# Optimization experiments

Measured on AMD Instinct MI355X. Metric: run time of the kernel, lower is better.

Reference implementation:

```python
import jax, jax.numpy as jnp
import numpy as np

EMBED_DIM = 1024
NUM_HEADS = 16
HEAD_DIM = EMBED_DIM // NUM_HEADS
TGT_LEN, BSZ = 2048, 4


def setup_inputs() -> dict:
    key = jax.random.key(0)
    ks = jax.random.split(key, 12)
    s = 1.0 / np.sqrt(EMBED_DIM)
    inp = {
        "query": jax.random.normal(ks[0], (TGT_LEN, BSZ, EMBED_DIM), jnp.float32),
        "key": jax.random.normal(ks[1], (TGT_LEN, BSZ, EMBED_DIM), jnp.float32),
        "value": jax.random.normal(ks[2], (TGT_LEN, BSZ, EMBED_DIM), jnp.float32),
        # nn.Linear weights: [out, in], y = x @ W.T + b
        "Wq": jax.random.normal(ks[3], (EMBED_DIM, EMBED_DIM), jnp.float32) * s,
        "bq": jax.random.normal(ks[4], (EMBED_DIM,), jnp.float32) * s,
        "Wk": jax.random.normal(ks[5], (EMBED_DIM, EMBED_DIM), jnp.float32) * s,
        "bk": jax.random.normal(ks[6], (EMBED_DIM,), jnp.float32) * s,
        "Wv": jax.random.normal(ks[7], (EMBED_DIM, EMBED_DIM), jnp.float32) * s,
        "bv": jax.random.normal(ks[8], (EMBED_DIM,), jnp.float32) * s,
        "Wo": jax.random.normal(ks[9], (EMBED_DIM, EMBED_DIM), jnp.float32) * s,
        "bo": jax.random.normal(ks[10], (EMBED_DIM,), jnp.float32) * s,
    }
    return inp


def _split_heads(x, seq_len, bsz):
    # [S, B, E] -> [B*H, S, Dh]
    return x.reshape(seq_len, bsz * NUM_HEADS, HEAD_DIM).transpose(1, 0, 2)


def reference(query, key, value, Wq, bq, Wk, bk, Wv, bv, Wo, bo):
    tgt_len, bsz, embed_dim = query.shape
    src_len = key.shape[0]
    q = query @ Wq.T + bq
    k = key @ Wk.T + bk
    v = value @ Wv.T + bv
    q = _split_heads(q, tgt_len, bsz)   # [B*H, T, Dh]
    k = _split_heads(k, src_len, bsz)   # [B*H, S, Dh]
    v = _split_heads(v, src_len, bsz)   # [B*H, S, Dh]
    scale = 1.0 / np.sqrt(HEAD_DIM).astype(np.float32)
    attn_weights = jnp.einsum('btd,bsd->bts', q, k) * scale  # [B*H, T, S]
    attn_weights = jax.nn.softmax(attn_weights, axis=-1)
    attn = jnp.einsum('bts,bsd->btd', attn_weights, v)       # [B*H, T, Dh]
    attn = attn.transpose(1, 0, 2).reshape(tgt_len, bsz, embed_dim)
    return attn @ Wo.T + bo
```

## Files before the change

kernel.cpp:

```cpp
#include <hip/hip_runtime.h>
#include <stdint.h>

#define TGT 2048
#define BSZQ 4
#define EMB 1024
#define NHEAD 16
#define DH 64
#define BH 64
#define MROWS 8192

using short8 = __attribute__((ext_vector_type(8))) short;
using f32x4  = __attribute__((ext_vector_type(4))) float;
typedef unsigned short u16;
typedef unsigned int u32;

#define QSCALE 0.18033688011112042f

__device__ __forceinline__ u16 f2bf(float f) {
  union { float f; u32 u; } v; v.f = f;
  return (u16)((v.u + 0x7fffu + ((v.u >> 16) & 1u)) >> 16);
}
__device__ __forceinline__ u32 packbf(float a, float b) {
  union { float f; u32 u; } x, y; x.f = a; y.f = b;
  return __builtin_amdgcn_perm(y.u + 0x8000u, x.u + 0x8000u, 0x07060302u);
}
__device__ __forceinline__ f32x4 mfma16(short8 a, short8 b, f32x4 c) {
  return __builtin_amdgcn_mfma_f32_16x16x32_bf16(a, b, c, 0, 0, 0);
}
__device__ __forceinline__ void gload_lds16(const u16* g, u16* l) {
  __builtin_amdgcn_global_load_lds((const __attribute__((address_space(1))) void*)g,
                                   (__attribute__((address_space(3))) void*)l,
                                   16, 0, 0);
}

__global__ __launch_bounds__(256)
void cvt3(const float* __restrict__ a, const float* __restrict__ b, const float* __restrict__ c,
          u16* __restrict__ oa, u16* __restrict__ ob, u16* __restrict__ oc)
{
  const float* s; u16* d;
  if (blockIdx.y == 0) { s = a; d = oa; }
  else if (blockIdx.y == 1) { s = b; d = ob; }
  else { s = c; d = oc; }
  const int i = (blockIdx.x * 256 + threadIdx.x) * 8;
  float4 v0 = *(const float4*)(s + i);
  float4 v1 = *(const float4*)(s + i + 4);
  union { u16 h[8]; short8 v; } r;
  r.h[0] = f2bf(v0.x); r.h[1] = f2bf(v0.y); r.h[2] = f2bf(v0.z); r.h[3] = f2bf(v0.w);
  r.h[4] = f2bf(v1.x); r.h[5] = f2bf(v1.y); r.h[6] = f2bf(v1.z); r.h[7] = f2bf(v1.w);
  *(short8*)(d + i) = r.v;
}
__global__ __launch_bounds__(256)
void cvt4(const float* __restrict__ a, const float* __restrict__ b,
          const float* __restrict__ c, const float* __restrict__ e,
          u16* __restrict__ oa, u16* __restrict__ ob, u16* __restrict__ oc, u16* __restrict__ oe)
{
  const float* s; u16* d;
  if (blockIdx.y == 0) { s = a; d = oa; }
  else if (blockIdx.y == 1) { s = b; d = ob; }
  else if (blockIdx.y == 2) { s = c; d = oc; }
  else { s = e; d = oe; }
  const int i = (blockIdx.x * 256 + threadIdx.x) * 8;
  float4 v0 = *(const float4*)(s + i);
  float4 v1 = *(const float4*)(s + i + 4);
  union { u16 h[8]; short8 v; } r;
  r.h[0] = f2bf(v0.x); r.h[1] = f2bf(v0.y); r.h[2] = f2bf(v0.z); r.h[3] = f2bf(v0.w);
  r.h[4] = f2bf(v1.x); r.h[5] = f2bf(v1.y); r.h[6] = f2bf(v1.z); r.h[7] = f2bf(v1.w);
  *(short8*)(d + i) = r.v;
}

__device__ __forceinline__
void gemm_body(const u16* __restrict__ A, const u16* __restrict__ W,
               const float* __restrict__ bias, void* __restrict__ outp,
               u16* As, u16* Bs, int mode, int m0, int n0)
{
  const int tid = threadIdx.x;
  const int wave = tid >> 6, lane = tid & 63;
  const int col16 = lane & 15, quad = lane >> 4;
  const int wr = (wave >> 1) * 64;
  const int wc = (wave & 1) * 64;
  const int sr = lane >> 3;
  const int sg = (lane & 7) ^ sr;
  const int fk = col16 & 7;

#define GSTAGE(K0) do { \
  _Pragma("unroll") for (int s_ = 0; s_ < 4; ++s_) \
    gload_lds16(A + (size_t)(m0 + wave * 32 + s_ * 8 + sr) * EMB + (K0) + sg * 8, \
                &As[(wave * 32 + s_ * 8) * 64]); \
  _Pragma("unroll") for (int s_ = 0; s_ < 4; ++s_) \
    gload_lds16(W + (size_t)(n0 + wave * 32 + s_ * 8 + sr) * EMB + (K0) + sg * 8, \
                &Bs[(wave * 32 + s_ * 8) * 64]); \
} while (0)

  f32x4 acc[4][4];
#pragma unroll
  for (int i = 0; i < 4; ++i)
#pragma unroll
    for (int j = 0; j < 4; ++j) acc[i][j] = (f32x4)0.0f;

  for (int kt = 0; kt < EMB / 64; ++kt) {
    if (kt) __syncthreads();
    GSTAGE(kt * 64);
    __syncthreads();
    short8 af[4][2], bfr[4][2];
#pragma unroll
    for (int kk = 0; kk < 2; ++kk) {
#pragma unroll
      for (int i = 0; i < 4; ++i)
        af[i][kk] = *(const short8*)&As[(wr + i * 16 + col16) * 64
                                        + (((kk * 4 + quad) ^ fk) << 3)];
#pragma unroll
      for (int j = 0; j < 4; ++j)
        bfr[j][kk] = *(const short8*)&Bs[(wc + j * 16 + col16) * 64
                                         + (((kk * 4 + quad) ^ fk) << 3)];
    }
#pragma unroll
    for (int i = 0; i < 4; ++i)
#pragma unroll
      for (int j = 0; j < 4; ++j) {
        acc[i][j] = mfma16(af[i][0], bfr[j][0], acc[i][j]);
        acc[i][j] = mfma16(af[i][1], bfr[j][1], acc[i][j]);
      }
  }
#undef GSTAGE

  const int rowb = quad * 4;
#pragma unroll
  for (int i = 0; i < 4; ++i) {
#pragma unroll
    for (int j = 0; j < 4; ++j) {
      const int gn = n0 + wc + j * 16 + col16;
      const float bia = bias[gn];
      const int h = gn >> 6, d = gn & 63;
#pragma unroll
      for (int r = 0; r < 4; ++r) {
        const int gm = m0 + wr + i * 16 + rowb + r;
        float val = acc[i][j][r] + bia;
        const int t = gm >> 2, b = gm & 3;
        if (mode == 0) {
          ((u16*)outp)[((size_t)(b * NHEAD + h) * TGT + t) * DH + d] = f2bf(val * QSCALE);
        } else if (mode == 1) {
          ((u16*)outp)[((size_t)(b * NHEAD + h) * TGT + t) * DH + d] = f2bf(val);
        } else if (mode == 2) {
          const int p = (t & ~63) + ((t & 12) << 2) + ((t & 48) >> 2) + (t & 3);
          ((u16*)outp)[((size_t)(b * NHEAD + h) * DH + d) * TGT + p] = f2bf(val);
        } else {
          ((float*)outp)[(size_t)gm * EMB + gn] = val;
        }
      }
    }
  }
}

__global__ __launch_bounds__(256, 4)
void gemm_qkv(const u16* __restrict__ qb, const u16* __restrict__ kb, const u16* __restrict__ vb,
              const u16* __restrict__ wq, const u16* __restrict__ wk, const u16* __restrict__ wv,
              const float* __restrict__ bq, const float* __restrict__ bk, const float* __restrict__ bv,
              u16* __restrict__ qh, u16* __restrict__ kh, u16* __restrict__ vtp)
{
  __shared__ u16 As[8192];
  __shared__ u16 Bs[8192];
  const int lin = ((int)blockIdx.z * 64 + blockIdx.y) * 8 + blockIdx.x;
  const int swz = (lin & 7) * 192 + (lin >> 3);
  const int n0 = (swz & 7) * 128;
  const int tmp = swz >> 3;
  const int m0 = (tmp & 63) * 128;
  const int z = tmp >> 6;
  const u16* A = (z == 0) ? qb : (z == 1) ? kb : vb;
  const u16* W = (z == 0) ? wq : (z == 1) ? wk : wv;
  const float* bias = (z == 0) ? bq : (z == 1) ? bk : bv;
  void* outp = (z == 0) ? (void*)qh : (z == 1) ? (void*)kh : (void*)vtp;
  gemm_body(A, W, bias, outp, As, Bs, z, m0, n0);
}

__global__ __launch_bounds__(256, 4)
void gemm_o(const u16* __restrict__ A, const u16* __restrict__ W,
            const float* __restrict__ bias, float* __restrict__ outp)
{
  __shared__ u16 As[8192];
  __shared__ u16 Bs[8192];
  const int lin = (int)blockIdx.y * 8 + blockIdx.x;
  const int swz = (lin & 7) * 64 + (lin >> 3);
  const int n0 = (swz & 7) * 128;
  const int m0 = (swz >> 3) * 128;
  gemm_body(A, W, bias, (void*)outp, As, Bs, 3, m0, n0);
}

__global__ __launch_bounds__(256, 4)
void flash_attn(const u16* __restrict__ qh, const u16* __restrict__ kh,
                const u16* __restrict__ vtp, u16* __restrict__ ao)
{
  __shared__ u16 Ks[2 * 64 * 64];
  __shared__ u16 Vs[2 * 64 * 64];

  const int tid = threadIdx.x;
  const int wave = tid >> 6, lane = tid & 63;
  const int col16 = lane & 15, quad = lane >> 4;
  const int id = blockIdx.x;
  const int bh = (id & 7) * 8 + (id >> 7);
  const int q0 = ((id >> 3) & 15) * 128;
  const int wq0 = q0 + wave * 32;

  const u16* qbase = qh + (size_t)bh * TGT * DH;
  const u16* kbase = kh + (size_t)bh * TGT * DH;
  const u16* vbase = vtp + (size_t)bh * DH * TGT;

  const int krl = lane >> 3;
  const int kgl = (lane & 7) ^ krl;

#define STAGE(S0, B) do { \
  _Pragma("unroll") for (int t_ = 0; t_ < 2; ++t_) { \
    gload_lds16(kbase + (size_t)((S0) + t_ * 32 + wave * 8 + krl) * DH + kgl * 8, \
                &Ks[(B) * 4096 + (t_ * 32 + wave * 8) * 64]); \
    gload_lds16(vbase + (size_t)(t_ * 32 + wave * 8 + krl) * TGT + (S0) + kgl * 8, \
                &Vs[(B) * 4096 + (t_ * 32 + wave * 8) * 64]); \
  } } while (0)

  short8 qf[2][2];
#pragma unroll
  for (int i = 0; i < 2; ++i)
#pragma unroll
    for (int kk = 0; kk < 2; ++kk)
      qf[i][kk] = *(const short8*)(qbase + (size_t)(wq0 + i * 16 + col16) * DH + kk * 32 + quad * 8);

  f32x4 oacc[2][4];
  float lsum[2];
#pragma unroll
  for (int i = 0; i < 2; ++i) {
    lsum[i] = 0.0f;
#pragma unroll
    for (int j = 0; j < 4; ++j) oacc[i][j] = (f32x4)0.0f;
  }

  STAGE(0, 0);

  for (int st = 0; st < TGT / 64; ++st) {
    const int cb = st & 1;
    __syncthreads();
    if (st < TGT / 64 - 1) STAGE((st + 1) * 64, cb ^ 1);

    u32 pka[4][2][2];
#pragma unroll
    for (int j = 0; j < 4; ++j) {
      const int R = j * 16 + col16;
      short8 kf0 = *(const short8*)&Ks[cb * 4096 + R * 64 + ((quad ^ (col16 & 7)) << 3)];
      short8 kf1 = *(const short8*)&Ks[cb * 4096 + R * 64 + (((quad + 4) ^ (col16 & 7)) << 3)];
#pragma unroll
      for (int i = 0; i < 2; ++i) {
        f32x4 t0 = mfma16(kf0, qf[i][0], (f32x4)0.0f);
        f32x4 s  = mfma16(kf1, qf[i][1], t0);
        float p0 = __builtin_amdgcn_exp2f(s[0]);
        float p1 = __builtin_amdgcn_exp2f(s[1]);
        float p2 = __builtin_amdgcn_exp2f(s[2]);
        float p3 = __builtin_amdgcn_exp2f(s[3]);
        lsum[i] += (p0 + p1) + (p2 + p3);
        pka[j][i][0] = packbf(p0, p1);
        pka[j][i][1] = packbf(p2, p3);
      }
    }
#pragma unroll
    for (int jd = 0; jd < 4; ++jd) {
      const int d = jd * 16 + col16;
#pragma unroll
      for (int h = 0; h < 2; ++h) {
        short8 vf = *(const short8*)&Vs[cb * 4096 + d * 64
                                        + (((quad * 2 + h) ^ (d & 7)) << 3)];
#pragma unroll
        for (int i = 0; i < 2; ++i) {
          union { u32 u[4]; short8 s8; } pa;
          pa.u[0] = pka[2 * h][i][0];     pa.u[1] = pka[2 * h][i][1];
          pa.u[2] = pka[2 * h + 1][i][0]; pa.u[3] = pka[2 * h + 1][i][1];
          oacc[i][jd] = mfma16(pa.s8, vf, oacc[i][jd]);
        }
      }
    }
  }
#undef STAGE

  float lrow[2][4];
#pragma unroll
  for (int i = 0; i < 2; ++i) {
    float L = lsum[i];
    L += __shfl_xor(L, 16, 64);
    L += __shfl_xor(L, 32, 64);
    L = __builtin_amdgcn_rcpf(L);
#pragma unroll
    for (int r = 0; r < 4; ++r) lrow[i][r] = __shfl(L, quad * 4 + r, 64);
  }
  const int b = bh >> 4, h = bh & 15;
#pragma unroll
  for (int i = 0; i < 2; ++i)
#pragma unroll
    for (int jd = 0; jd < 4; ++jd)
#pragma unroll
      for (int r = 0; r < 4; ++r) {
        const int t = q0 + wave * 32 + i * 16 + quad * 4 + r;
        const int d = jd * 16 + col16;
        ao[((size_t)t * BSZQ + b) * EMB + h * DH + d] = f2bf(oacc[i][jd][r] * lrow[i][r]);
      }
}

extern "C" void kernel_launch(void* const* d_in, const int* in_sizes, int n_in,
                              void* d_out, int out_size, void* d_ws, size_t ws_size,
                              hipStream_t stream) {
  const float* query = (const float*)d_in[0];
  const float* key   = (const float*)d_in[1];
  const float* value = (const float*)d_in[2];
  const float* Wq = (const float*)d_in[3];
  const float* bq = (const float*)d_in[4];
  const float* Wk = (const float*)d_in[5];
  const float* bk = (const float*)d_in[6];
  const float* Wv = (const float*)d_in[7];
  const float* bv = (const float*)d_in[8];
  const float* Wo = (const float*)d_in[9];
  const float* bo = (const float*)d_in[10];

  const size_t BIG = (size_t)MROWS * EMB;
  const size_t WSZ = (size_t)EMB * EMB;
  u16* buf0 = (u16*)d_ws;
  u16* buf1 = buf0 + BIG;
  u16* buf2 = buf1 + BIG;
  u16* buf3 = buf2 + BIG;
  u16* wqb  = buf3 + BIG;
  u16* wkb  = wqb + WSZ;
  u16* wvb  = wkb + WSZ;
  u16* wob  = wvb + WSZ;
  u16* khs  = (u16*)d_out;
  u16* vts  = khs + BIG;

  cvt3<<<dim3(BIG / 2048, 3), 256, 0, stream>>>(query, key, value, buf0, buf1, buf2);
  cvt4<<<dim3(WSZ / 2048, 4), 256, 0, stream>>>(Wq, Wk, Wv, Wo, wqb, wkb, wvb, wob);

  gemm_qkv<<<dim3(EMB / 128, MROWS / 128, 3), 256, 0, stream>>>(
      buf0, buf1, buf2, wqb, wkb, wvb, bq, bk, bv,
      buf3 , khs , vts );

  flash_attn<<<1024, 256, 0, stream>>>(buf3, khs, vts, buf2);

  gemm_o<<<dim3(EMB / 128, MROWS / 128), 256, 0, stream>>>(buf2, wob, bo, (float*)d_out);
}
```

Baseline: 360.2 us.

## Double-buffer GEMM LDS tiles with K=32 stages and fragment-ordered layout

The shared GEMM body now splits K into 32-wide stages held in two LDS buffers. It issues the global-to-LDS load for the next stage before computing the current one, so each iteration needs one barrier instead of two. The LDS layout changes from XOR-swizzled 64-wide rows to 16x32 fragment-ordered blocks, so each lane reads its MFMA operand directly without swizzle arithmetic. This costs twice as many loop iterations with half the MFMAs each. The new read pattern may also behave differently for bank conflicts, and correctness depends on the async load completing before the barrier.

```diff
diff --git a/kernel.cpp b/kernel.cpp
--- a/kernel.cpp
+++ b/kernel.cpp
@@ -78,18 +78,19 @@
   const int col16 = lane & 15, quad = lane >> 4;
   const int wr = (wave >> 1) * 64;
   const int wc = (wave & 1) * 64;
-  const int sr = lane >> 3;
-  const int sg = (lane & 7) ^ sr;
-  const int fk = col16 & 7;
-
-#define GSTAGE(K0) do { \
-  _Pragma("unroll") for (int s_ = 0; s_ < 4; ++s_) \
-    gload_lds16(A + (size_t)(m0 + wave * 32 + s_ * 8 + sr) * EMB + (K0) + sg * 8, \
-                &As[(wave * 32 + s_ * 8) * 64]); \
-  _Pragma("unroll") for (int s_ = 0; s_ < 4; ++s_) \
-    gload_lds16(W + (size_t)(n0 + wave * 32 + s_ * 8 + sr) * EMB + (K0) + sg * 8, \
-                &Bs[(wave * 32 + s_ * 8) * 64]); \
-} while (0)
+  const int sr16 = lane & 15;
+  const int sl = lane >> 4;
+  const int akb = (wave >> 1) * 4;
+  const int bkb = (wave & 1) * 4;
+
+#define GSTAGE(K0, CB) do { \
+  _Pragma("unroll") for (int s_ = 0; s_ < 2; ++s_) { \
+    const int t_ = wave * 2 + s_; \
+    gload_lds16(A + (size_t)(m0 + t_ * 16 + sr16) * EMB + (K0) + sl * 8, \
+                &As[(CB) * 4096 + t_ * 512]); \
+    gload_lds16(W + (size_t)(n0 + t_ * 16 + sr16) * EMB + (K0) + sl * 8, \
+                &Bs[(CB) * 4096 + t_ * 512]); \
+  } } while (0)
 
   f32x4 acc[4][4];
 #pragma unroll
@@ -97,29 +98,23 @@
 #pragma unroll
     for (int j = 0; j < 4; ++j) acc[i][j] = (f32x4)0.0f;
 
-  for (int kt = 0; kt < EMB / 64; ++kt) {
-    if (kt) __syncthreads();
-    GSTAGE(kt * 64);
+  GSTAGE(0, 0);
+  for (int kt = 0; kt < EMB / 32; ++kt) {
+    const int cb = kt & 1;
     __syncthreads();
-    short8 af[4][2], bfr[4][2];
-#pragma unroll
-    for (int kk = 0; kk < 2; ++kk) {
-#pragma unroll
-      for (int i = 0; i < 4; ++i)
-        af[i][kk] = *(const short8*)&As[(wr + i * 16 + col16) * 64
-                                        + (((kk * 4 + quad) ^ fk) << 3)];
+    if (kt < EMB / 32 - 1) GSTAGE((kt + 1) * 32, cb ^ 1);
+    short8 af[4], bfr[4];
+#pragma unroll
+    for (int i = 0; i < 4; ++i)
+      af[i] = *(const short8*)&As[cb * 4096 + (akb + i) * 512 + quad * 128 + col16 * 8];
+#pragma unroll
+    for (int j = 0; j < 4; ++j)
+      bfr[j] = *(const short8*)&Bs[cb * 4096 + (bkb + j) * 512 + quad * 128 + col16 * 8];
+#pragma unroll
+    for (int i = 0; i < 4; ++i)
 #pragma unroll
       for (int j = 0; j < 4; ++j)
-        bfr[j][kk] = *(const short8*)&Bs[(wc + j * 16 + col16) * 64
-                                         + (((kk * 4 + quad) ^ fk) << 3)];
-    }
-#pragma unroll
-    for (int i = 0; i < 4; ++i)
-#pragma unroll
-      for (int j = 0; j < 4; ++j) {
-        acc[i][j] = mfma16(af[i][0], bfr[j][0], acc[i][j]);
-        acc[i][j] = mfma16(af[i][1], bfr[j][1], acc[i][j]);
-      }
+        acc[i][j] = mfma16(af[i], bfr[j], acc[i][j]);
   }
 #undef GSTAGE
 
@@ -157,8 +152,8 @@
               const float* __restrict__ bq, const float* __restrict__ bk, const float* __restrict__ bv,
               u16* __restrict__ qh, u16* __restrict__ kh, u16* __restrict__ vtp)
 {
-  __shared__ u16 As[8192];
-  __shared__ u16 Bs[8192];
+  __shared__ u16 As[2 * 4096];
+  __shared__ u16 Bs[2 * 4096];
   const int lin = ((int)blockIdx.z * 64 + blockIdx.y) * 8 + blockIdx.x;
   const int swz = (lin & 7) * 192 + (lin >> 3);
   const int n0 = (swz & 7) * 128;
@@ -176,8 +171,8 @@
 void gemm_o(const u16* __restrict__ A, const u16* __restrict__ W,
             const float* __restrict__ bias, float* __restrict__ outp)
 {
-  __shared__ u16 As[8192];
-  __shared__ u16 Bs[8192];
+  __shared__ u16 As[2 * 4096];
+  __shared__ u16 Bs[2 * 4096];
   const int lin = (int)blockIdx.y * 8 + blockIdx.x;
   const int swz = (lin & 7) * 64 + (lin >> 3);
   const int n0 = (swz & 7) * 128;
```

New measurement: 404.2 us. +12.2%, slower.

## Use 256x128 QKV GEMM tiles with 512 threads and merge conversion kernels

Applied to the files above, without the earlier changes.

Merges the two fp32-to-bf16 conversion kernels into one launch, with weight blocks beyond their size exiting early. The QKV projection GEMM moves to 256x128 tiles with 8 waves per block, halving the block count and reusing each staged weight tile across more rows. Its LDS layout changes to 16-row sub-tiles without the XOR swizzle, which may bring bank conflicts back. The larger block also uses more LDS and drops the 4-blocks-per-CU launch bound, which can lower occupancy.

```diff
diff --git a/kernel.cpp b/kernel.cpp
--- a/kernel.cpp
+++ b/kernel.cpp
@@ -34,95 +34,38 @@
 }
 
 __global__ __launch_bounds__(256)
-void cvt3(const float* __restrict__ a, const float* __restrict__ b, const float* __restrict__ c,
-          u16* __restrict__ oa, u16* __restrict__ ob, u16* __restrict__ oc)
-{
+void cvt_all(const float* __restrict__ q, const float* __restrict__ k, const float* __restrict__ v,
+             const float* __restrict__ wq, const float* __restrict__ wk,
+             const float* __restrict__ wv, const float* __restrict__ wo,
+             u16* __restrict__ oq, u16* __restrict__ ok, u16* __restrict__ ov,
+             u16* __restrict__ owq, u16* __restrict__ owk, u16* __restrict__ owv,
+             u16* __restrict__ owo)
+{
+  const int y = blockIdx.y;
+  if (y >= 3 && blockIdx.x >= 512) return;
   const float* s; u16* d;
-  if (blockIdx.y == 0) { s = a; d = oa; }
-  else if (blockIdx.y == 1) { s = b; d = ob; }
-  else { s = c; d = oc; }
+  switch (y) {
+    case 0: s = q;  d = oq;  break;
+    case 1: s = k;  d = ok;  break;
+    case 2: s = v;  d = ov;  break;
+    case 3: s = wq; d = owq; break;
+    case 4: s = wk; d = owk; break;
+    case 5: s = wv; d = owv; break;
+    default: s = wo; d = owo; break;
+  }
   const int i = (blockIdx.x * 256 + threadIdx.x) * 8;
   float4 v0 = *(const float4*)(s + i);
   float4 v1 = *(const float4*)(s + i + 4);
-  union { u16 h[8]; short8 v; } r;
+  union { u16 h[8]; short8 vv; } r;
   r.h[0] = f2bf(v0.x); r.h[1] = f2bf(v0.y); r.h[2] = f2bf(v0.z); r.h[3] = f2bf(v0.w);
   r.h[4] = f2bf(v1.x); r.h[5] = f2bf(v1.y); r.h[6] = f2bf(v1.z); r.h[7] = f2bf(v1.w);
-  *(short8*)(d + i) = r.v;
-}
-__global__ __launch_bounds__(256)
-void cvt4(const float* __restrict__ a, const float* __restrict__ b,
-          const float* __restrict__ c, const float* __restrict__ e,
-          u16* __restrict__ oa, u16* __restrict__ ob, u16* __restrict__ oc, u16* __restrict__ oe)
-{
-  const float* s; u16* d;
-  if (blockIdx.y == 0) { s = a; d = oa; }
-  else if (blockIdx.y == 1) { s = b; d = ob; }
-  else if (blockIdx.y == 2) { s = c; d = oc; }
-  else { s = e; d = oe; }
-  const int i = (blockIdx.x * 256 + threadIdx.x) * 8;
-  float4 v0 = *(const float4*)(s + i);
-  float4 v1 = *(const float4*)(s + i + 4);
-  union { u16 h[8]; short8 v; } r;
-  r.h[0] = f2bf(v0.x); r.h[1] = f2bf(v0.y); r.h[2] = f2bf(v0.z); r.h[3] = f2bf(v0.w);
-  r.h[4] = f2bf(v1.x); r.h[5] = f2bf(v1.y); r.h[6] = f2bf(v1.z); r.h[7] = f2bf(v1.w);
-  *(short8*)(d + i) = r.v;
+  *(short8*)(d + i) = r.vv;
 }
 
 __device__ __forceinline__
-void gemm_body(const u16* __restrict__ A, const u16* __restrict__ W,
-               const float* __restrict__ bias, void* __restrict__ outp,
-               u16* As, u16* Bs, int mode, int m0, int n0)
-{
-  const int tid = threadIdx.x;
-  const int wave = tid >> 6, lane = tid & 63;
-  const int col16 = lane & 15, quad = lane >> 4;
-  const int wr = (wave >> 1) * 64;
-  const int wc = (wave & 1) * 64;
-  const int sr = lane >> 3;
-  const int sg = (lane & 7) ^ sr;
-  const int fk = col16 & 7;
-
-#define GSTAGE(K0) do { \
-  _Pragma("unroll") for (int s_ = 0; s_ < 4; ++s_) \
-    gload_lds16(A + (size_t)(m0 + wave * 32 + s_ * 8 + sr) * EMB + (K0) + sg * 8, \
-                &As[(wave * 32 + s_ * 8) * 64]); \
-  _Pragma("unroll") for (int s_ = 0; s_ < 4; ++s_) \
-    gload_lds16(W + (size_t)(n0 + wave * 32 + s_ * 8 + sr) * EMB + (K0) + sg * 8, \
-                &Bs[(wave * 32 + s_ * 8) * 64]); \
-} while (0)
-
-  f32x4 acc[4][4];
-#pragma unroll
-  for (int i = 0; i < 4; ++i)
-#pragma unroll
-    for (int j = 0; j < 4; ++j) acc[i][j] = (f32x4)0.0f;
-
-  for (int kt = 0; kt < EMB / 64; ++kt) {
-    if (kt) __syncthreads();
-    GSTAGE(kt * 64);
-    __syncthreads();
-    short8 af[4][2], bfr[4][2];
-#pragma unroll
-    for (int kk = 0; kk < 2; ++kk) {
-#pragma unroll
-      for (int i = 0; i < 4; ++i)
-        af[i][kk] = *(const short8*)&As[(wr + i * 16 + col16) * 64
-                                        + (((kk * 4 + quad) ^ fk) << 3)];
-#pragma unroll
-      for (int j = 0; j < 4; ++j)
-        bfr[j][kk] = *(const short8*)&Bs[(wc + j * 16 + col16) * 64
-                                         + (((kk * 4 + quad) ^ fk) << 3)];
-    }
-#pragma unroll
-    for (int i = 0; i < 4; ++i)
-#pragma unroll
-      for (int j = 0; j < 4; ++j) {
-        acc[i][j] = mfma16(af[i][0], bfr[j][0], acc[i][j]);
-        acc[i][j] = mfma16(af[i][1], bfr[j][1], acc[i][j]);
-      }
-  }
-#undef GSTAGE
-
+void gemm_epilogue(f32x4 acc[4][4], const float* __restrict__ bias, void* __restrict__ outp,
+                   int mode, int m0, int n0, int wr, int wc, int col16, int quad)
+{
   const int rowb = quad * 4;
 #pragma unroll
   for (int i = 0; i < 4; ++i) {
@@ -151,25 +94,79 @@
   }
 }
 
-__global__ __launch_bounds__(256, 4)
+__global__ __launch_bounds__(512)
 void gemm_qkv(const u16* __restrict__ qb, const u16* __restrict__ kb, const u16* __restrict__ vb,
               const u16* __restrict__ wq, const u16* __restrict__ wk, const u16* __restrict__ wv,
               const float* __restrict__ bq, const float* __restrict__ bk, const float* __restrict__ bv,
               u16* __restrict__ qh, u16* __restrict__ kh, u16* __restrict__ vtp)
 {
-  __shared__ u16 As[8192];
+  __shared__ u16 As[16384];
   __shared__ u16 Bs[8192];
-  const int lin = ((int)blockIdx.z * 64 + blockIdx.y) * 8 + blockIdx.x;
-  const int swz = (lin & 7) * 192 + (lin >> 3);
+
+  const int lin = ((int)blockIdx.z * 32 + blockIdx.y) * 8 + blockIdx.x;
+  const int swz = (lin & 7) * 96 + (lin >> 3);
   const int n0 = (swz & 7) * 128;
   const int tmp = swz >> 3;
-  const int m0 = (tmp & 63) * 128;
-  const int z = tmp >> 6;
+  const int m0 = (tmp & 31) * 256;
+  const int z = tmp >> 5;
   const u16* A = (z == 0) ? qb : (z == 1) ? kb : vb;
   const u16* W = (z == 0) ? wq : (z == 1) ? wk : wv;
   const float* bias = (z == 0) ? bq : (z == 1) ? bk : bv;
   void* outp = (z == 0) ? (void*)qh : (z == 1) ? (void*)kh : (void*)vtp;
-  gemm_body(A, W, bias, outp, As, Bs, z, m0, n0);
+
+  const int tid = threadIdx.x;
+  const int wave = tid >> 6, lane = tid & 63;
+  const int col16 = lane & 15, quad = lane >> 4;
+  const int wr = (wave >> 1) * 64;
+  const int wc = (wave & 1) * 64;
+  const int sr = lane & 15;
+  const int sq = lane >> 4;
+
+#define GSTAGE(K0) do { \
+  _Pragma("unroll") for (int g_ = 0; g_ < 2; ++g_) { \
+    const int t_ = wave * 2 + g_; \
+    _Pragma("unroll") for (int h_ = 0; h_ < 2; ++h_) \
+      gload_lds16(A + (size_t)(m0 + t_ * 16 + sr) * EMB + (K0) + (h_ * 4 + sq) * 8, \
+                  &As[t_ * 1024 + h_ * 512]); \
+  } \
+  _Pragma("unroll") for (int h_ = 0; h_ < 2; ++h_) \
+    gload_lds16(W + (size_t)(n0 + wave * 16 + sr) * EMB + (K0) + (h_ * 4 + sq) * 8, \
+                &Bs[wave * 1024 + h_ * 512]); \
+} while (0)
+
+  f32x4 acc[4][4];
+#pragma unroll
+  for (int i = 0; i < 4; ++i)
+#pragma unroll
+    for (int j = 0; j < 4; ++j) acc[i][j] = (f32x4)0.0f;
+
+  for (int kt = 0; kt < EMB / 64; ++kt) {
+    if (kt) __syncthreads();
+    GSTAGE(kt * 64);
+    __syncthreads();
+    short8 af[4][2], bfr[4][2];
+#pragma unroll
+    for (int kk = 0; kk < 2; ++kk) {
+#pragma unroll
+      for (int i = 0; i < 4; ++i)
+        af[i][kk] = *(const short8*)&As[((wave >> 1) * 4 + i) * 1024
+                                        + ((kk * 4 + quad) * 16 + col16) * 8];
+#pragma unroll
+      for (int j = 0; j < 4; ++j)
+        bfr[j][kk] = *(const short8*)&Bs[((wave & 1) * 4 + j) * 1024
+                                         + ((kk * 4 + quad) * 16 + col16) * 8];
+    }
+#pragma unroll
+    for (int i = 0; i < 4; ++i)
+#pragma unroll
+      for (int j = 0; j < 4; ++j) {
+        acc[i][j] = mfma16(af[i][0], bfr[j][0], acc[i][j]);
+        acc[i][j] = mfma16(af[i][1], bfr[j][1], acc[i][j]);
+      }
+  }
+#undef GSTAGE
+
+  gemm_epilogue(acc, bias, outp, z, m0, n0, wr, wc, col16, quad);
 }
 
 __global__ __launch_bounds__(256, 4)
@@ -182,7 +179,58 @@
   const int swz = (lin & 7) * 64 + (lin >> 3);
   const int n0 = (swz & 7) * 128;
   const int m0 = (swz >> 3) * 128;
-  gemm_body(A, W, bias, (void*)outp, As, Bs, 3, m0, n0);
+
+  const int tid = threadIdx.x;
+  const int wave = tid >> 6, lane = tid & 63;
+  const int col16 = lane & 15, quad = lane >> 4;
+  const int wr = (wave >> 1) * 64;
+  const int wc = (wave & 1) * 64;
+  const int sr = lane >> 3;
+  const int sg = (lane & 7) ^ sr;
+  const int fk = col16 & 7;
+
+#define GSTAGE(K0) do { \
+  _Pragma("unroll") for (int s_ = 0; s_ < 4; ++s_) \
+    gload_lds16(A + (size_t)(m0 + wave * 32 + s_ * 8 + sr) * EMB + (K0) + sg * 8, \
+                &As[(wave * 32 + s_ * 8) * 64]); \
+  _Pragma("unroll") for (int s_ = 0; s_ < 4; ++s_) \
+    gload_lds16(W + (size_t)(n0 + wave * 32 + s_ * 8 + sr) * EMB + (K0) + sg * 8, \
+                &Bs[(wave * 32 + s_ * 8) * 64]); \
+} while (0)
+
+  f32x4 acc[4][4];
+#pragma unroll
+  for (int i = 0; i < 4; ++i)
+#pragma unroll
+    for (int j = 0; j < 4; ++j) acc[i][j] = (f32x4)0.0f;
+
+  for (int kt = 0; kt < EMB / 64; ++kt) {
+    if (kt) __syncthreads();
+    GSTAGE(kt * 64);
+    __syncthreads();
+    short8 af[4][2], bfr[4][2];
+#pragma unroll
+    for (int kk = 0; kk < 2; ++kk) {
+#pragma unroll
+      for (int i = 0; i < 4; ++i)
+        af[i][kk] = *(const short8*)&As[(wr + i * 16 + col16) * 64
+                                        + (((kk * 4 + quad) ^ fk) << 3)];
+#pragma unroll
+      for (int j = 0; j < 4; ++j)
+        bfr[j][kk] = *(const short8*)&Bs[(wc + j * 16 + col16) * 64
+                                         + (((kk * 4 + quad) ^ fk) << 3)];
+    }
+#pragma unroll
+    for (int i = 0; i < 4; ++i)
+#pragma unroll
+      for (int j = 0; j < 4; ++j) {
+        acc[i][j] = mfma16(af[i][0], bfr[j][0], acc[i][j]);
+        acc[i][j] = mfma16(af[i][1], bfr[j][1], acc[i][j]);
+      }
+  }
+#undef GSTAGE
+
+  gemm_epilogue(acc, bias, (void*)outp, 3, m0, n0, wr, wc, col16, quad);
 }
 
 __global__ __launch_bounds__(256, 4)
@@ -327,10 +375,11 @@
   u16* khs  = (u16*)d_out;
   u16* vts  = khs + BIG;
 
-  cvt3<<<dim3(BIG / 2048, 3), 256, 0, stream>>>(query, key, value, buf0, buf1, buf2);
-  cvt4<<<dim3(WSZ / 2048, 4), 256, 0, stream>>>(Wq, Wk, Wv, Wo, wqb, wkb, wvb, wob);
-
-  gemm_qkv<<<dim3(EMB / 128, MROWS / 128, 3), 256, 0, stream>>>(
+  cvt_all<<<dim3(BIG / 2048, 7), 256, 0, stream>>>(
+      query, key, value, Wq, Wk, Wv, Wo,
+      buf0, buf1, buf2, wqb, wkb, wvb, wob);
+
+  gemm_qkv<<<dim3(EMB / 128, MROWS / 256, 3), 512, 0, stream>>>(
       buf0, buf1, buf2, wqb, wkb, wvb, bq, bk, bv,
       buf3 , khs , vts );
 
```

Measured after the change: 381.2 us. 5.8% more time.
